# Kernel tuning notes

Hardware: AMD Instinct MI355X
Metric: run time of the kernel (lower is better)

Reference implementation:

```python
import jax, jax.numpy as jnp
import numpy as np

B, L, D, H, NL = 4, 2048, 128, 4, 2
DH = D // H
FF = 2 * D
EPS_LN = 1e-5


def _p(key, shape, scale=0.05):
    return (jax.random.normal(key, shape, dtype=jnp.float32) * scale)


def setup_inputs() -> dict:
    key = jax.random.key(0)
    ks = jax.random.split(key, 40)
    inp = {
        "local_global": jax.random.normal(ks[0], (B, D), dtype=jnp.float32),
        "task_features": jax.random.normal(ks[1], (B, L, 15), dtype=jnp.float32),
        "privacy_features": jax.random.normal(ks[2], (B, L, 6), dtype=jnp.float32),
        "dag_features": jax.random.normal(ks[3], (B, L, 4), dtype=jnp.float32),
        # float mask in [0,1); values > 0.5 are MASKED (set to -inf) per torch code
        "attn_mask": jax.random.uniform(ks[4], (B, L, L), dtype=jnp.float32),
        # input projections (stored [in, out]; torch Linear does x @ W.T + b)
        "task_W": _p(ks[5], (15, D)), "task_b": jnp.zeros((D,), jnp.float32),
        "priv_W": _p(ks[6], (6, D)), "priv_b": jnp.zeros((D,), jnp.float32),
        "dag_W": _p(ks[7], (4, D)), "dag_b": jnp.zeros((D,), jnp.float32),
        "pre_g": jnp.ones((D,), jnp.float32), "pre_b": jnp.zeros((D,), jnp.float32),
        "post_g": jnp.ones((D,), jnp.float32), "post_b": jnp.zeros((D,), jnp.float32),
        "out_W": _p(ks[8], (D, D)), "out_b": jnp.zeros((D,), jnp.float32),
        # per-layer params stacked on leading NL axis
        "qW": _p(ks[9], (NL, D, D)), "qb": jnp.zeros((NL, D), jnp.float32),
        "kW": _p(ks[10], (NL, D, D)), "kb": jnp.zeros((NL, D), jnp.float32),
        "vW": _p(ks[11], (NL, D, D)), "vb": jnp.zeros((NL, D), jnp.float32),
        "oW": _p(ks[12], (NL, D, D)), "ob": jnp.zeros((NL, D), jnp.float32),
        "n1g": jnp.ones((NL, D), jnp.float32), "n1b": jnp.zeros((NL, D), jnp.float32),
        "n2g": jnp.ones((NL, D), jnp.float32), "n2b": jnp.zeros((NL, D), jnp.float32),
        "f1W": _p(ks[13], (NL, D, FF)), "f1b": jnp.zeros((NL, FF), jnp.float32),
        "f2W": _p(ks[14], (NL, FF, D)), "f2b": jnp.zeros((NL, D), jnp.float32),
    }
    return inp


def _layernorm(x, g, b):
    mu = x.mean(-1, keepdims=True)
    var = ((x - mu) ** 2).mean(-1, keepdims=True)
    return (x - mu) * jax.lax.rsqrt(var + EPS_LN) * g + b


def _attention(x, add_mask, Wq, bq, Wk, bk, Wv, bv, Wo, bo):
    # x: [B,L,D]; add_mask: [B,L,L] additive (0 or -inf)
    def heads(y):
        return y.reshape(B, L, H, DH).transpose(0, 2, 1, 3)  # [B,H,L,DH]
    q = heads(x @ Wq + bq)
    k = heads(x @ Wk + bk)
    v = heads(x @ Wv + bv)
    scale = 1.0 / np.sqrt(DH).astype(np.float32)
    scores = jnp.einsum('bhqd,bhkd->bhqk', q, k) * scale + add_mask[:, None]
    # fully-masked-row diagonal fixup (torch: set diag score to 0 where row max is -inf)
    row_max = scores.max(-1)                       # [B,H,L]
    fully_masked = jnp.isinf(row_max) & (row_max < 0)
    eye = jnp.eye(L, dtype=bool)
    scores = jnp.where(fully_masked[..., None] & eye, 0.0, scores)
    w = jax.nn.softmax(scores, axis=-1)
    # NaN fallback: if any NaN, replace with 1/L and renormalize (applied globally, as torch does)
    has_nan = jnp.isnan(w).any()
    fixed = jnp.nan_to_num(w, nan=1.0 / L)
    fixed = fixed / (fixed.sum(-1, keepdims=True) + 1e-8)
    w = jnp.where(has_nan, fixed, w)
    out = jnp.einsum('bhqk,bhkd->bhqd', w, v)      # [B,H,L,DH]
    out = out.transpose(0, 2, 1, 3).reshape(B, L, D)
    return out @ Wo + bo


def reference(local_global, task_features, privacy_features, dag_features, attn_mask,
              task_W, task_b, priv_W, priv_b, dag_W, dag_b,
              pre_g, pre_b, post_g, post_b, out_W, out_b,
              qW, qb, kW, kb, vW, vb, oW, ob,
              n1g, n1b, n2g, n2b, f1W, f1b, f2W, f2b):
    # normalize mask: >0.5 means masked; fix all-False rows by masking their diagonal (torch quirk)
    mb = attn_mask > 0.5                            # [B,L,L] bool, True = mask out
    need_fix = ~mb.any(-1)                          # [B,L]
    eye = jnp.eye(L, dtype=bool)
    mb = mb | (need_fix[..., None] & eye)
    add_mask = jnp.where(mb, -jnp.inf, 0.0).astype(jnp.float32)

    ctx = (task_features @ task_W + task_b) + (privacy_features @ priv_W + priv_b) \
          + (dag_features @ dag_W + dag_b)
    x = _layernorm(ctx, pre_g, pre_b)
    for i in range(NL):  # eval mode: dropout = identity
        sa = _attention(_layernorm(x, n1g[i], n1b[i]), add_mask,
                        qW[i], qb[i], kW[i], kb[i], vW[i], vb[i], oW[i], ob[i])
        x = x + sa
        h = _layernorm(x, n2g[i], n2b[i])
        ff = jax.nn.gelu(h @ f1W[i] + f1b[i], approximate=False) @ f2W[i] + f2b[i]
        x = x + ff
    enc = _layernorm(x, post_g, post_b)
    global_ctx = enc.mean(axis=1)                   # [B,D]
    fused = global_ctx + 0.1 * local_global
    aligned = fused @ out_W + out_b
    return aligned
```

## Files before the change

kernel.cpp:

```cpp
#include <hip/hip_runtime.h>
#include <hip/hip_bf16.h>

#define DEV __device__ __forceinline__

typedef float f32x4 __attribute__((ext_vector_type(4)));
typedef float f32x16 __attribute__((ext_vector_type(16)));
typedef short s16x8 __attribute__((ext_vector_type(8)));
typedef __bf16 bf16x8 __attribute__((ext_vector_type(8)));

DEV bf16x8 as_bf16(s16x8 v) { return __builtin_bit_cast(bf16x8, v); }

DEV unsigned short f2bf(float f) {
    union { __hip_bfloat16 h; unsigned short u; } c;
    c.h = __float2bfloat16(f);
    return c.u;
}

DEV unsigned f2bf2(float lo, float hi) {
    unsigned ulo = __builtin_bit_cast(unsigned, lo);
    unsigned uhi = __builtin_bit_cast(unsigned, hi);
    ulo = (ulo + 0x7fffu + ((ulo >> 16) & 1u)) >> 16;
    uhi = (uhi + 0x7fffu + ((uhi >> 16) & 1u)) & 0xffff0000u;
    return ulo | uhi;
}

DEV float wave_sum64(float v) {
#pragma unroll
    for (int m = 1; m < 64; m <<= 1) v += __shfl_xor(v, m, 64);
    return v;
}

DEV int swz8(int row) { return ((row ^ (row >> 3)) & 7) << 4; }

constexpr float QSCL = (float)(1.4426950408889634 / 5.656854249492381);

__global__ __launch_bounds__(256) void gace_mask_k(
    const float* __restrict__ am, unsigned long long* __restrict__ bits)
{
    const int tid = threadIdx.x, wid = tid >> 6, l = tid & 63;
    const int row = blockIdx.x * 4 + wid;
    const float* mrow = am + (size_t)row * 2048;
    unsigned long long myword = 0, orAll = 0, andAll = ~0ull;
#pragma unroll 4
    for (int w = 0; w < 32; ++w) {
        unsigned long long bal = __ballot(mrow[w * 64 + l] > 0.5f);
        if (w == l) myword = bal;
        orAll |= bal; andAll &= bal;
    }
    const int lrow = row & 2047;
    const int dw = lrow >> 6, dbit = lrow & 63;
    if (l == dw) {
        if (orAll == 0ull) myword |= (1ull << dbit);
        else if (andAll == ~0ull) myword &= ~(1ull << dbit);
    }
    if (l < 32) bits[(size_t)row * 32 + l] = myword;
}

__global__ __launch_bounds__(256) void gace_prep_k(
    const float* __restrict__ qW, const float* __restrict__ kW,
    const float* __restrict__ vW, const float* __restrict__ oW,
    const float* __restrict__ f1W, const float* __restrict__ f2W,
    const float* __restrict__ qb, const float* __restrict__ kb,
    const float* __restrict__ vb,
    unsigned short* __restrict__ wbf, float* __restrict__ bcat)
{
    const int y = blockIdx.y;
    const int idx = blockIdx.x * 256 + threadIdx.x;
    if (y == 6) {
        if (idx < 2 * 384) {
            const int i = idx / 384, j = idx % 384;
            float v;
            if (j < 128)      v = qb[i * 128 + j] * QSCL;
            else if (j < 256) v = kb[i * 128 + j - 128];
            else              v = vb[i * 128 + j - 256];
            bcat[idx] = v;
        }
        return;
    }
    const float* src; int K_, N_, off; float scl = 1.0f;
    switch (y) {
        case 0:  src = qW;  K_ = 128; N_ = 128; off = 0;      scl = QSCL; break;
        case 1:  src = kW;  K_ = 128; N_ = 128; off = 16384;  break;
        case 2:  src = vW;  K_ = 128; N_ = 128; off = 32768;  break;
        case 3:  src = oW;  K_ = 128; N_ = 128; off = 49152;  break;
        case 4:  src = f1W; K_ = 128; N_ = 256; off = 65536;  break;
        default: src = f2W; K_ = 256; N_ = 128; off = 98304;  break;
    }
    const int per = K_ * N_;
    if (idx >= 2 * per) return;
    const int i = idx / per, rem = idx % per;
    const int n = rem / K_, k = rem % K_;
    wbf[(size_t)i * 131072 + off + n * K_ + k] = f2bf(src[(size_t)i * per + k * N_ + n] * scl);
}

__global__ __launch_bounds__(256) void gace_ctxln_k(
    const float* __restrict__ task, const float* __restrict__ priv, const float* __restrict__ dag,
    const float* __restrict__ tW, const float* __restrict__ tb,
    const float* __restrict__ pW, const float* __restrict__ pb,
    const float* __restrict__ dW, const float* __restrict__ db,
    const float* __restrict__ gam, const float* __restrict__ bet,
    float* __restrict__ x)
{
    const int tid = threadIdx.x, wid = tid >> 6, l = tid & 63;
    const int row = blockIdx.x * 4 + wid;
    const int d0 = l, d1 = l + 64;
    float a0 = tb[d0] + pb[d0] + db[d0];
    float a1 = tb[d1] + pb[d1] + db[d1];
    const float* tf = task + (size_t)row * 15;
#pragma unroll
    for (int j = 0; j < 15; ++j) { const float t = tf[j]; a0 += t * tW[j * 128 + d0]; a1 += t * tW[j * 128 + d1]; }
    const float* pf = priv + (size_t)row * 6;
#pragma unroll
    for (int j = 0; j < 6; ++j) { const float t = pf[j]; a0 += t * pW[j * 128 + d0]; a1 += t * pW[j * 128 + d1]; }
    const float* df = dag + (size_t)row * 4;
#pragma unroll
    for (int j = 0; j < 4; ++j) { const float t = df[j]; a0 += t * dW[j * 128 + d0]; a1 += t * dW[j * 128 + d1]; }
    const float s = wave_sum64(a0 + a1);
    const float mean = s * (1.f / 128.f);
    const float e0 = a0 - mean, e1 = a1 - mean;
    const float s2 = wave_sum64(e0 * e0 + e1 * e1);
    const float rs = rsqrtf(s2 * (1.f / 128.f) + 1e-5f);
    x[(size_t)row * 128 + d0] = e0 * rs * gam[d0] + bet[d0];
    x[(size_t)row * 128 + d1] = e1 * rs * gam[d1] + bet[d1];
}

template<int PRO, int EPI, int KD>
__global__ __launch_bounds__(256) void gace_mega_k(
    const unsigned short* __restrict__ A, int lda,
    const float* __restrict__ xin,
    const float* __restrict__ Op, const float* __restrict__ ml,
    const float* __restrict__ gam, const float* __restrict__ bet,
    const unsigned short* __restrict__ Wt,
    const float* __restrict__ bias,
    unsigned short* __restrict__ outb, int ldo,
    float* __restrict__ xadd)
{
    const int tid = threadIdx.x;
    const int wid = tid >> 6, l = tid & 63;
    const int g = (l >> 4) & 3, c16 = l & 15;
    const int m0 = blockIdx.x * 64 + wid * 16;
    const int n0 = blockIdx.y * 64;
    const int arow = m0 + c16;
    constexpr int NKC = KD / 32;

    s16x8 af[NKC];
    if (PRO == 0) {
#pragma unroll
        for (int kc = 0; kc < NKC; ++kc)
            af[kc] = *(const s16x8*)&A[(size_t)arow * lda + kc * 32 + 8 * g];
    } else if (PRO == 1) {
        float v[4][8];
#pragma unroll
        for (int kc = 0; kc < 4; ++kc) {
            const f32x4 a0 = *(const f32x4*)&xin[(size_t)arow * 128 + kc * 32 + 8 * g];
            const f32x4 a1 = *(const f32x4*)&xin[(size_t)arow * 128 + kc * 32 + 8 * g + 4];
#pragma unroll
            for (int e = 0; e < 4; ++e) { v[kc][e] = a0[e]; v[kc][4 + e] = a1[e]; }
        }
        float s = 0.f;
#pragma unroll
        for (int kc = 0; kc < 4; ++kc)
#pragma unroll
            for (int e = 0; e < 8; ++e) s += v[kc][e];
        s += __shfl_xor(s, 16, 64); s += __shfl_xor(s, 32, 64);
        const float mean = s * (1.f / 128.f);
        float s2 = 0.f;
#pragma unroll
        for (int kc = 0; kc < 4; ++kc)
#pragma unroll
            for (int e = 0; e < 8; ++e) { const float d = v[kc][e] - mean; s2 += d * d; }
        s2 += __shfl_xor(s2, 16, 64); s2 += __shfl_xor(s2, 32, 64);
        const float rs = rsqrtf(s2 * (1.f / 128.f) + 1e-5f);
#pragma unroll
        for (int kc = 0; kc < 4; ++kc) {
            union { s16x8 v8; unsigned d[4]; } pk;
#pragma unroll
            for (int j = 0; j < 4; ++j) {
                const int col = kc * 32 + 8 * g + 2 * j;
                const float x0 = (v[kc][2 * j] - mean) * rs * gam[col] + bet[col];
                const float x1 = (v[kc][2 * j + 1] - mean) * rs * gam[col + 1] + bet[col + 1];
                pk.d[j] = f2bf2(x0, x1);
            }
            af[kc] = pk.v8;
        }
    } else {
#pragma unroll
        for (int kc = 0; kc < 4; ++kc) {
            float o[8];
#pragma unroll
            for (int e = 0; e < 8; ++e) o[e] = 0.f;
            float Ls = 0.f;
#pragma unroll
            for (int sp = 0; sp < 4; ++sp) {
                const size_t ro = (size_t)sp * 8192 + arow;
                const f32x4 a0 = *(const f32x4*)&Op[ro * 128 + kc * 32 + 8 * g];
                const f32x4 a1 = *(const f32x4*)&Op[ro * 128 + kc * 32 + 8 * g + 4];
#pragma unroll
                for (int e = 0; e < 4; ++e) { o[e] += a0[e]; o[4 + e] += a1[e]; }
                Ls += ml[ro * 4 + kc];
            }
            const float inv = 1.f / Ls;
            union { s16x8 v8; unsigned d[4]; } pk;
#pragma unroll
            for (int j = 0; j < 4; ++j) pk.d[j] = f2bf2(o[2 * j] * inv, o[2 * j + 1] * inv);
            af[kc] = pk.v8;
        }
    }

    f32x4 acc[4];
#pragma unroll
    for (int i = 0; i < 4; ++i) acc[i] = f32x4{0.f, 0.f, 0.f, 0.f};
#pragma unroll
    for (int ns = 0; ns < 4; ++ns) {
        const unsigned short* wrow = Wt + (size_t)(n0 + 16 * ns + c16) * KD;
#pragma unroll
        for (int kc = 0; kc < NKC; ++kc) {
            const s16x8 bfv = *(const s16x8*)&wrow[kc * 32 + 8 * g];
            acc[ns] = __builtin_amdgcn_mfma_f32_16x16x32_bf16(
                as_bf16(af[kc]), as_bf16(bfv), acc[ns], 0, 0, 0);
        }
    }
#pragma unroll
    for (int ns = 0; ns < 4; ++ns) {
        const int n = n0 + ns * 16 + c16;
        const float bv = bias[n];
#pragma unroll
        for (int r = 0; r < 4; ++r) {
            const int row = m0 + 4 * g + r;
            float v = acc[ns][r] + bv;
            if (EPI == 1) v = v * 0.5f * (1.0f + erff(v * 0.70710678118654752f));
            if (EPI == 2) xadd[(size_t)row * 128 + n] += v;
            else          outb[(size_t)row * ldo + n] = f2bf(v);
        }
    }
}

__global__ __launch_bounds__(256) void gace_flash4_k(
    const unsigned short* __restrict__ QKV,
    const unsigned long long* __restrict__ bits,
    float* __restrict__ Op, float* __restrict__ ml)
{
    __shared__ __align__(16) unsigned short Ks[64 * 40];
    __shared__ __align__(16) char VtB[32 * 128];

    const int tid = threadIdx.x;
    const int wid = tid >> 6, l = tid & 63;
    const int c32 = l & 31, hi = l >> 5;
    const int bid = blockIdx.x;
    const int split = bid & 3, qc = (bid >> 2) & 15, h = (bid >> 6) & 3, b = bid >> 8;
    const size_t base = (size_t)b * 2048;
    const int qb0 = qc * 128 + wid * 32;
    const int q = qb0 + c32;

    const unsigned short* qrow = &QKV[(base + q) * 384 + h * 32];
    const s16x8 qf0 = *(const s16x8*)&qrow[8 * hi];
    const s16x8 qf1 = *(const s16x8*)&qrow[16 + 8 * hi];

    f32x16 oacc, zv;
#pragma unroll
    for (int i = 0; i < 16; ++i) { oacc[i] = 0.f; zv[i] = 0.f; }
    float l_ = 0.f;

    const int sr = tid >> 2;
    const int se = (tid & 3) << 3;
    const int lowr = sr & 31, t12 = lowr & 12;
    const int prow = (sr & 32) | (((t12 == 4) | (t12 == 8)) ? (lowr ^ 12) : lowr);
    unsigned short* kdst = &Ks[prow * 40 + se];
    int voff[8];
#pragma unroll
    for (int j = 0; j < 8; ++j) {
        const int row = se + j;
        voff[j] = row * 128 + ((2 * sr) ^ swz8(row));
    }
    const int vswz = swz8(c32);
    const unsigned short* kbase = &QKV[base * 384 + 128 + h * 32 + se];
    const unsigned short* vbase = kbase + 128;
    const unsigned long long* bq = &bits[(base + q) * 32 + split * 8];

    const int kv0 = split * 512;
    s16x8 kreg = *(const s16x8*)&kbase[(size_t)(kv0 + sr) * 384];
    s16x8 vreg = *(const s16x8*)&vbase[(size_t)(kv0 + sr) * 384];
    unsigned long long wb = bq[0];
    *(s16x8*)kdst = kreg;
    {
        union { s16x8 v; unsigned short u[8]; } vv; vv.v = vreg;
#pragma unroll
        for (int j = 0; j < 8; ++j) *(unsigned short*)&VtB[voff[j]] = vv.u[j];
    }
    __syncthreads();

    for (int t = 0; t < 8; ++t) {
        unsigned long long wbn = 0;
        if (t < 7) {
            const int kvn = kv0 + (t + 1) * 64;
            kreg = *(const s16x8*)&kbase[(size_t)(kvn + sr) * 384];
            vreg = *(const s16x8*)&vbase[(size_t)(kvn + sr) * 384];
            wbn = bq[t + 1];
        }
        const unsigned long long wbs = wb >> (8 * hi);
        const unsigned wlo = (unsigned)wbs, whiw = (unsigned)(wbs >> 32);
#pragma unroll
        for (int H = 0; H < 2; ++H) {
            const unsigned short* krow = &Ks[(32 * H + c32) * 40 + 8 * hi];
            f32x16 sac = __builtin_amdgcn_mfma_f32_32x32x16_bf16(
                as_bf16(*(const s16x8*)&krow[0]), as_bf16(qf0), zv, 0, 0, 0);
            sac = __builtin_amdgcn_mfma_f32_32x32x16_bf16(
                as_bf16(*(const s16x8*)&krow[16]), as_bf16(qf1), sac, 0, 0, 0);
            const unsigned word = (H == 0) ? wlo : whiw;
#pragma unroll
            for (int ch = 0; ch < 2; ++ch) {
                const int c = 2 * H + ch;
                const int bb = ch * 16;
                float p[8];
#pragma unroll
                for (int e = 0; e < 8; ++e) {
                    const float pe = exp2f(sac[ch * 8 + e]);
                    p[e] = ((word >> (bb + e)) & 1u) ? 0.f : pe;
                }
                l_ += ((p[0] + p[1]) + (p[2] + p[3])) + ((p[4] + p[5]) + (p[6] + p[7]));
                union { s16x8 v; unsigned d[4]; } pa;
#pragma unroll
                for (int j = 0; j < 4; ++j)
                    asm("v_cvt_pk_bf16_f32 %0, %1, %2"
                        : "=v"(pa.d[j]) : "v"(p[2 * j]), "v"(p[2 * j + 1]));
                const s16x8 vf = *(const s16x8*)&VtB[c32 * 128 + ((32 * c + 16 * hi) ^ vswz)];
                oacc = __builtin_amdgcn_mfma_f32_32x32x16_bf16(
                    as_bf16(pa.v), as_bf16(vf), oacc, 0, 0, 0);
            }
        }
        if (t < 7) {
            __syncthreads();
            *(s16x8*)kdst = kreg;
            union { s16x8 v; unsigned short u[8]; } vv; vv.v = vreg;
#pragma unroll
            for (int j = 0; j < 8; ++j) *(unsigned short*)&VtB[voff[j]] = vv.u[j];
            __syncthreads();
            wb = wbn;
        }
    }
    l_ += __shfl_xor(l_, 32, 64);
    float* orow = &Op[((size_t)split * 8192 + base + qb0) * 128 + h * 32 + c32];
#pragma unroll
    for (int r = 0; r < 16; ++r) {
        const int qoff = (r & 3) + 8 * (r >> 2) + 4 * hi;
        orow[(size_t)qoff * 128] = oacc[r];
    }
    if (l < 32) ml[((size_t)split * 8192 + base + q) * 4 + h] = l_;
}

__global__ __launch_bounds__(256) void gace_tailA_k(
    const float* __restrict__ x, const float* __restrict__ gam, const float* __restrict__ bet,
    float* __restrict__ partial)
{
    const int tid = threadIdx.x, wid = tid >> 6, l = tid & 63;
    const int row0 = blockIdx.x * 64 + wid * 16;
    const float g0 = gam[l], g1v = gam[l + 64], b0 = bet[l], b1 = bet[l + 64];
    float a0 = 0.f, a1 = 0.f;
    for (int rr = 0; rr < 16; ++rr) {
        const float* xr = x + (size_t)(row0 + rr) * 128;
        const float v0 = xr[l], v1 = xr[l + 64];
        const float s = wave_sum64(v0 + v1);
        const float mean = s * (1.f / 128.f);
        const float d0 = v0 - mean, d1 = v1 - mean;
        const float s2 = wave_sum64(d0 * d0 + d1 * d1);
        const float rs = rsqrtf(s2 * (1.f / 128.f) + 1e-5f);
        a0 += d0 * rs * g0 + b0;
        a1 += d1 * rs * g1v + b1;
    }
    __shared__ float red[4][128];
    red[wid][l] = a0;
    red[wid][l + 64] = a1;
    __syncthreads();
    if (tid < 128) {
        partial[(size_t)blockIdx.x * 128 + tid] =
            red[0][tid] + red[1][tid] + red[2][tid] + red[3][tid];
    }
}

__global__ __launch_bounds__(128) void gace_tailB_k(
    const float* __restrict__ partial, const float* __restrict__ lg,
    const float* __restrict__ oW, const float* __restrict__ obv,
    float* __restrict__ out)
{
    const int tid = threadIdx.x;
    __shared__ float fused[4][128];
#pragma unroll
    for (int b2 = 0; b2 < 4; ++b2) {
        float s = 0.f;
        for (int c = 0; c < 32; ++c) s += partial[(size_t)(b2 * 32 + c) * 128 + tid];
        fused[b2][tid] = s * (1.f / 2048.f) + 0.1f * lg[b2 * 128 + tid];
    }
    __syncthreads();
#pragma unroll
    for (int b2 = 0; b2 < 4; ++b2) {
        float r = obv[tid];
        for (int d2 = 0; d2 < 128; ++d2) r += fused[b2][d2] * oW[d2 * 128 + tid];
        out[b2 * 128 + tid] = r;
    }
}

extern "C" void kernel_launch(void* const* d_in, const int* in_sizes, int n_in,
                              void* d_out, int out_size, void* d_ws, size_t ws_size,
                              hipStream_t stream)
{
    (void)in_sizes; (void)n_in; (void)out_size; (void)ws_size;
    const float* local_global = (const float*)d_in[0];
    const float* task   = (const float*)d_in[1];
    const float* priv   = (const float*)d_in[2];
    const float* dag    = (const float*)d_in[3];
    const float* amask  = (const float*)d_in[4];
    const float* task_W = (const float*)d_in[5];
    const float* task_b = (const float*)d_in[6];
    const float* priv_W = (const float*)d_in[7];
    const float* priv_b = (const float*)d_in[8];
    const float* dag_W  = (const float*)d_in[9];
    const float* dag_b  = (const float*)d_in[10];
    const float* pre_g  = (const float*)d_in[11];
    const float* pre_b  = (const float*)d_in[12];
    const float* post_g = (const float*)d_in[13];
    const float* post_b = (const float*)d_in[14];
    const float* out_W  = (const float*)d_in[15];
    const float* out_b  = (const float*)d_in[16];
    const float* qW = (const float*)d_in[17];
    const float* qb = (const float*)d_in[18];
    const float* kW = (const float*)d_in[19];
    const float* kb = (const float*)d_in[20];
    const float* vW = (const float*)d_in[21];
    const float* vb = (const float*)d_in[22];
    const float* oW = (const float*)d_in[23];
    const float* ob = (const float*)d_in[24];
    const float* n1g = (const float*)d_in[25];
    const float* n1b = (const float*)d_in[26];
    const float* n2g = (const float*)d_in[27];
    const float* n2b = (const float*)d_in[28];
    const float* f1W = (const float*)d_in[29];
    const float* f1b = (const float*)d_in[30];
    const float* f2W = (const float*)d_in[31];
    const float* f2b = (const float*)d_in[32];

    char* ws = (char*)d_ws;
    size_t off = 0;
    auto carve = [&](size_t sz) {
        void* p = ws + off;
        off += (sz + 255) & ~(size_t)255;
        return p;
    };
    unsigned long long* bits = (unsigned long long*)carve(8192ull * 32 * 8);
    float*          x    = (float*)carve(8192ull * 128 * 4);
    unsigned short* qkv  = (unsigned short*)carve(8192ull * 384 * 2);
    unsigned short* g1   = (unsigned short*)carve(8192ull * 256 * 2);
    float*          part = (float*)carve(128ull * 128 * 4);
    float*          Op   = (float*)carve(4ull * 8192 * 128 * 4);
    float*          mlb  = (float*)carve(4ull * 8192 * 4 * 4);
    unsigned short* wbf  = (unsigned short*)carve(2ull * 131072 * 2);
    float*          bcat = (float*)carve(2ull * 384 * 4);

    gace_prep_k<<<dim3(256, 7), 256, 0, stream>>>(qW, kW, vW, oW, f1W, f2W,
                                                  qb, kb, vb, wbf, bcat);
    gace_mask_k<<<2048, 256, 0, stream>>>(amask, bits);
    gace_ctxln_k<<<2048, 256, 0, stream>>>(task, priv, dag, task_W, task_b,
                                           priv_W, priv_b, dag_W, dag_b,
                                           pre_g, pre_b, x);
    for (int i = 0; i < 2; ++i) {
        const unsigned short* wl = wbf + (size_t)i * 131072;
        gace_mega_k<1, 0, 128><<<dim3(128, 6), 256, 0, stream>>>(
            nullptr, 0, x, nullptr, nullptr, n1g + i * 128, n1b + i * 128,
            wl, bcat + i * 384, qkv, 384, nullptr);
        gace_flash4_k<<<1024, 256, 0, stream>>>(qkv, bits, Op, mlb);
        gace_mega_k<2, 2, 128><<<dim3(128, 2), 256, 0, stream>>>(
            nullptr, 0, nullptr, Op, mlb, nullptr, nullptr,
            wl + 49152, ob + i * 128, nullptr, 0, x);
        gace_mega_k<1, 1, 128><<<dim3(128, 4), 256, 0, stream>>>(
            nullptr, 0, x, nullptr, nullptr, n2g + i * 128, n2b + i * 128,
            wl + 65536, f1b + i * 256, g1, 256, nullptr);
        gace_mega_k<0, 2, 256><<<dim3(128, 2), 256, 0, stream>>>(
            g1, 256, nullptr, nullptr, nullptr, nullptr, nullptr,
            wl + 98304, f2b + i * 128, nullptr, 0, x);
    }
    gace_tailA_k<<<128, 256, 0, stream>>>(x, post_g, post_b, part);
    gace_tailB_k<<<1, 128, 0, stream>>>(part, local_global, out_W, out_b, (float*)d_out);
}
```

Measured before the change: 189.1 us.

## Write V transposed from QKV GEMM and drop LDS staging in flash attention

The QKV projection epilogue now writes V in a transposed [head_dim, token] layout and Q/K into a narrower buffer. The flash attention kernel then reads K and V fragments straight from global memory, with no LDS staging and no per-tile barriers. The mask, context-layernorm and weight-prep kernels are also merged into a single launch to cut launch overhead. The risk is that direct global loads of K/V per wave, without shared-memory reuse, may add memory traffic and latency that the removed barriers do not make up for.

```diff
diff --git a/kernel.cpp b/kernel.cpp
--- a/kernel.cpp
+++ b/kernel.cpp
@@ -6,6 +6,7 @@
 typedef float f32x4 __attribute__((ext_vector_type(4)));
 typedef float f32x16 __attribute__((ext_vector_type(16)));
 typedef short s16x8 __attribute__((ext_vector_type(8)));
+typedef unsigned short u16x4 __attribute__((ext_vector_type(4)));
 typedef __bf16 bf16x8 __attribute__((ext_vector_type(8)));
 
 DEV bf16x8 as_bf16(s16x8 v) { return __builtin_bit_cast(bf16x8, v); }
@@ -30,33 +31,16 @@
     return v;
 }
 
-DEV int swz8(int row) { return ((row ^ (row >> 3)) & 7) << 4; }
-
 constexpr float QSCL = (float)(1.4426950408889634 / 5.656854249492381);
 
-__global__ __launch_bounds__(256) void gace_mask_k(
-    const float* __restrict__ am, unsigned long long* __restrict__ bits)
-{
-    const int tid = threadIdx.x, wid = tid >> 6, l = tid & 63;
-    const int row = blockIdx.x * 4 + wid;
-    const float* mrow = am + (size_t)row * 2048;
-    unsigned long long myword = 0, orAll = 0, andAll = ~0ull;
-#pragma unroll 4
-    for (int w = 0; w < 32; ++w) {
-        unsigned long long bal = __ballot(mrow[w * 64 + l] > 0.5f);
-        if (w == l) myword = bal;
-        orAll |= bal; andAll &= bal;
-    }
-    const int lrow = row & 2047;
-    const int dw = lrow >> 6, dbit = lrow & 63;
-    if (l == dw) {
-        if (orAll == 0ull) myword |= (1ull << dbit);
-        else if (andAll == ~0ull) myword &= ~(1ull << dbit);
-    }
-    if (l < 32) bits[(size_t)row * 32 + l] = myword;
-}
-
-__global__ __launch_bounds__(256) void gace_prep_k(
+__global__ __launch_bounds__(256) void gace_setup_k(
+    const float* __restrict__ am, unsigned long long* __restrict__ bits,
+    const float* __restrict__ task, const float* __restrict__ priv, const float* __restrict__ dag,
+    const float* __restrict__ tW, const float* __restrict__ tb,
+    const float* __restrict__ pW, const float* __restrict__ pb,
+    const float* __restrict__ dW, const float* __restrict__ db,
+    const float* __restrict__ pre_g, const float* __restrict__ pre_b,
+    float* __restrict__ x,
     const float* __restrict__ qW, const float* __restrict__ kW,
     const float* __restrict__ vW, const float* __restrict__ oW,
     const float* __restrict__ f1W, const float* __restrict__ f2W,
@@ -64,8 +48,53 @@
     const float* __restrict__ vb,
     unsigned short* __restrict__ wbf, float* __restrict__ bcat)
 {
-    const int y = blockIdx.y;
-    const int idx = blockIdx.x * 256 + threadIdx.x;
+    const int bx = blockIdx.x;
+    const int tid = threadIdx.x, wid = tid >> 6, l = tid & 63;
+    if (bx < 2048) {
+        const int row = bx * 4 + wid;
+        const float* mrow = am + (size_t)row * 2048;
+        unsigned long long myword = 0, orAll = 0, andAll = ~0ull;
+#pragma unroll 4
+        for (int w = 0; w < 32; ++w) {
+            unsigned long long bal = __ballot(mrow[w * 64 + l] > 0.5f);
+            if (w == l) myword = bal;
+            orAll |= bal; andAll &= bal;
+        }
+        const int lrow = row & 2047;
+        const int dw = lrow >> 6, dbit = lrow & 63;
+        if (l == dw) {
+            if (orAll == 0ull) myword |= (1ull << dbit);
+            else if (andAll == ~0ull) myword &= ~(1ull << dbit);
+        }
+        if (l < 32) bits[(size_t)row * 32 + l] = myword;
+        return;
+    }
+    if (bx < 4096) {
+        const int row = (bx - 2048) * 4 + wid;
+        const int d0 = l, d1 = l + 64;
+        float a0 = tb[d0] + pb[d0] + db[d0];
+        float a1 = tb[d1] + pb[d1] + db[d1];
+        const float* tf = task + (size_t)row * 15;
+#pragma unroll
+        for (int j = 0; j < 15; ++j) { const float t = tf[j]; a0 += t * tW[j * 128 + d0]; a1 += t * tW[j * 128 + d1]; }
+        const float* pf = priv + (size_t)row * 6;
+#pragma unroll
+        for (int j = 0; j < 6; ++j) { const float t = pf[j]; a0 += t * pW[j * 128 + d0]; a1 += t * pW[j * 128 + d1]; }
+        const float* df = dag + (size_t)row * 4;
+#pragma unroll
+        for (int j = 0; j < 4; ++j) { const float t = df[j]; a0 += t * dW[j * 128 + d0]; a1 += t * dW[j * 128 + d1]; }
+        const float s = wave_sum64(a0 + a1);
+        const float mean = s * (1.f / 128.f);
+        const float e0 = a0 - mean, e1 = a1 - mean;
+        const float s2 = wave_sum64(e0 * e0 + e1 * e1);
+        const float rs = rsqrtf(s2 * (1.f / 128.f) + 1e-5f);
+        x[(size_t)row * 128 + d0] = e0 * rs * pre_g[d0] + pre_b[d0];
+        x[(size_t)row * 128 + d1] = e1 * rs * pre_g[d1] + pre_b[d1];
+        return;
+    }
+    const int bx2 = bx - 4096;
+    const int y = bx2 >> 8;
+    const int idx = (bx2 & 255) * 256 + tid;
     if (y == 6) {
         if (idx < 2 * 384) {
             const int i = idx / 384, j = idx % 384;
@@ -91,37 +120,6 @@
     const int i = idx / per, rem = idx % per;
     const int n = rem / K_, k = rem % K_;
     wbf[(size_t)i * 131072 + off + n * K_ + k] = f2bf(src[(size_t)i * per + k * N_ + n] * scl);
-}
-
-__global__ __launch_bounds__(256) void gace_ctxln_k(
-    const float* __restrict__ task, const float* __restrict__ priv, const float* __restrict__ dag,
-    const float* __restrict__ tW, const float* __restrict__ tb,
-    const float* __restrict__ pW, const float* __restrict__ pb,
-    const float* __restrict__ dW, const float* __restrict__ db,
-    const float* __restrict__ gam, const float* __restrict__ bet,
-    float* __restrict__ x)
-{
-    const int tid = threadIdx.x, wid = tid >> 6, l = tid & 63;
-    const int row = blockIdx.x * 4 + wid;
-    const int d0 = l, d1 = l + 64;
-    float a0 = tb[d0] + pb[d0] + db[d0];
-    float a1 = tb[d1] + pb[d1] + db[d1];
-    const float* tf = task + (size_t)row * 15;
-#pragma unroll
-    for (int j = 0; j < 15; ++j) { const float t = tf[j]; a0 += t * tW[j * 128 + d0]; a1 += t * tW[j * 128 + d1]; }
-    const float* pf = priv + (size_t)row * 6;
-#pragma unroll
-    for (int j = 0; j < 6; ++j) { const float t = pf[j]; a0 += t * pW[j * 128 + d0]; a1 += t * pW[j * 128 + d1]; }
-    const float* df = dag + (size_t)row * 4;
-#pragma unroll
-    for (int j = 0; j < 4; ++j) { const float t = df[j]; a0 += t * dW[j * 128 + d0]; a1 += t * dW[j * 128 + d1]; }
-    const float s = wave_sum64(a0 + a1);
-    const float mean = s * (1.f / 128.f);
-    const float e0 = a0 - mean, e1 = a1 - mean;
-    const float s2 = wave_sum64(e0 * e0 + e1 * e1);
-    const float rs = rsqrtf(s2 * (1.f / 128.f) + 1e-5f);
-    x[(size_t)row * 128 + d0] = e0 * rs * gam[d0] + bet[d0];
-    x[(size_t)row * 128 + d1] = e1 * rs * gam[d1] + bet[d1];
 }
 
 template<int PRO, int EPI, int KD>
@@ -133,7 +131,7 @@
     const unsigned short* __restrict__ Wt,
     const float* __restrict__ bias,
     unsigned short* __restrict__ outb, int ldo,
-    float* __restrict__ xadd)
+    float* __restrict__ xadd, unsigned short* __restrict__ vtbuf)
 {
     const int tid = threadIdx.x;
     const int wid = tid >> 6, l = tid & 63;
@@ -220,6 +218,19 @@
                 as_bf16(af[kc]), as_bf16(bfv), acc[ns], 0, 0, 0);
         }
     }
+    if (EPI == 0 && vtbuf != nullptr && n0 >= 256) {
+        const int row0 = m0 + 4 * g;
+#pragma unroll
+        for (int ns = 0; ns < 4; ++ns) {
+            const int n = n0 + ns * 16 + c16;
+            const float bv = bias[n];
+            u16x4 pk;
+#pragma unroll
+            for (int r = 0; r < 4; ++r) pk[r] = f2bf(acc[ns][r] + bv);
+            *(u16x4*)&vtbuf[(size_t)(n - 256) * 8192 + row0] = pk;
+        }
+        return;
+    }
 #pragma unroll
     for (int ns = 0; ns < 4; ++ns) {
         const int n = n0 + ns * 16 + c16;
@@ -235,14 +246,12 @@
     }
 }
 
-__global__ __launch_bounds__(256) void gace_flash4_k(
-    const unsigned short* __restrict__ QKV,
+__global__ __launch_bounds__(256) void gace_flash5_k(
+    const unsigned short* __restrict__ QK,
+    const unsigned short* __restrict__ Vt,
     const unsigned long long* __restrict__ bits,
     float* __restrict__ Op, float* __restrict__ ml)
 {
-    __shared__ __align__(16) unsigned short Ks[64 * 40];
-    __shared__ __align__(16) char VtB[32 * 128];
-
     const int tid = threadIdx.x;
     const int wid = tid >> 6, l = tid & 63;
     const int c32 = l & 31, hi = l >> 5;
@@ -252,60 +261,33 @@
     const int qb0 = qc * 128 + wid * 32;
     const int q = qb0 + c32;
 
-    const unsigned short* qrow = &QKV[(base + q) * 384 + h * 32];
+    const unsigned short* qrow = &QK[(base + q) * 256 + h * 32];
     const s16x8 qf0 = *(const s16x8*)&qrow[8 * hi];
     const s16x8 qf1 = *(const s16x8*)&qrow[16 + 8 * hi];
 
+    const int t12 = c32 & 12;
+    const int kvA = (t12 == 4 || t12 == 8) ? (c32 ^ 12) : c32;
+
     f32x16 oacc, zv;
 #pragma unroll
     for (int i = 0; i < 16; ++i) { oacc[i] = 0.f; zv[i] = 0.f; }
     float l_ = 0.f;
 
-    const int sr = tid >> 2;
-    const int se = (tid & 3) << 3;
-    const int lowr = sr & 31, t12 = lowr & 12;
-    const int prow = (sr & 32) | (((t12 == 4) | (t12 == 8)) ? (lowr ^ 12) : lowr);
-    unsigned short* kdst = &Ks[prow * 40 + se];
-    int voff[8];
-#pragma unroll
-    for (int j = 0; j < 8; ++j) {
-        const int row = se + j;
-        voff[j] = row * 128 + ((2 * sr) ^ swz8(row));
-    }
-    const int vswz = swz8(c32);
-    const unsigned short* kbase = &QKV[base * 384 + 128 + h * 32 + se];
-    const unsigned short* vbase = kbase + 128;
+    const int kv0 = split * 512;
     const unsigned long long* bq = &bits[(base + q) * 32 + split * 8];
-
-    const int kv0 = split * 512;
-    s16x8 kreg = *(const s16x8*)&kbase[(size_t)(kv0 + sr) * 384];
-    s16x8 vreg = *(const s16x8*)&vbase[(size_t)(kv0 + sr) * 384];
-    unsigned long long wb = bq[0];
-    *(s16x8*)kdst = kreg;
-    {
-        union { s16x8 v; unsigned short u[8]; } vv; vv.v = vreg;
-#pragma unroll
-        for (int j = 0; j < 8; ++j) *(unsigned short*)&VtB[voff[j]] = vv.u[j];
-    }
-    __syncthreads();
+    const unsigned short* kbase = &QK[(base + kv0) * 256 + 128 + h * 32 + 8 * hi];
+    const unsigned short* vtb = &Vt[(size_t)(h * 32 + c32) * 8192 + base + kv0 + 8 * hi];
 
     for (int t = 0; t < 8; ++t) {
-        unsigned long long wbn = 0;
-        if (t < 7) {
-            const int kvn = kv0 + (t + 1) * 64;
-            kreg = *(const s16x8*)&kbase[(size_t)(kvn + sr) * 384];
-            vreg = *(const s16x8*)&vbase[(size_t)(kvn + sr) * 384];
-            wbn = bq[t + 1];
-        }
-        const unsigned long long wbs = wb >> (8 * hi);
+        const unsigned long long wbs = bq[t] >> (8 * hi);
         const unsigned wlo = (unsigned)wbs, whiw = (unsigned)(wbs >> 32);
 #pragma unroll
         for (int H = 0; H < 2; ++H) {
-            const unsigned short* krow = &Ks[(32 * H + c32) * 40 + 8 * hi];
+            const unsigned short* kr = kbase + (size_t)(t * 64 + 32 * H + kvA) * 256;
             f32x16 sac = __builtin_amdgcn_mfma_f32_32x32x16_bf16(
-                as_bf16(*(const s16x8*)&krow[0]), as_bf16(qf0), zv, 0, 0, 0);
+                as_bf16(*(const s16x8*)&kr[0]), as_bf16(qf0), zv, 0, 0, 0);
             sac = __builtin_amdgcn_mfma_f32_32x32x16_bf16(
-                as_bf16(*(const s16x8*)&krow[16]), as_bf16(qf1), sac, 0, 0, 0);
+                as_bf16(*(const s16x8*)&kr[16]), as_bf16(qf1), sac, 0, 0, 0);
             const unsigned word = (H == 0) ? wlo : whiw;
 #pragma unroll
             for (int ch = 0; ch < 2; ++ch) {
@@ -323,19 +305,10 @@
                 for (int j = 0; j < 4; ++j)
                     asm("v_cvt_pk_bf16_f32 %0, %1, %2"
                         : "=v"(pa.d[j]) : "v"(p[2 * j]), "v"(p[2 * j + 1]));
-                const s16x8 vf = *(const s16x8*)&VtB[c32 * 128 + ((32 * c + 16 * hi) ^ vswz)];
+                const s16x8 vf = *(const s16x8*)&vtb[t * 64 + 16 * c];
                 oacc = __builtin_amdgcn_mfma_f32_32x32x16_bf16(
                     as_bf16(pa.v), as_bf16(vf), oacc, 0, 0, 0);
             }
-        }
-        if (t < 7) {
-            __syncthreads();
-            *(s16x8*)kdst = kreg;
-            union { s16x8 v; unsigned short u[8]; } vv; vv.v = vreg;
-#pragma unroll
-            for (int j = 0; j < 8; ++j) *(unsigned short*)&VtB[voff[j]] = vv.u[j];
-            __syncthreads();
-            wb = wbn;
         }
     }
     l_ += __shfl_xor(l_, 32, 64);
@@ -447,7 +420,8 @@
     };
     unsigned long long* bits = (unsigned long long*)carve(8192ull * 32 * 8);
     float*          x    = (float*)carve(8192ull * 128 * 4);
-    unsigned short* qkv  = (unsigned short*)carve(8192ull * 384 * 2);
+    unsigned short* qk   = (unsigned short*)carve(8192ull * 256 * 2);
+    unsigned short* vt   = (unsigned short*)carve(128ull * 8192 * 2);
     unsigned short* g1   = (unsigned short*)carve(8192ull * 256 * 2);
     float*          part = (float*)carve(128ull * 128 * 4);
     float*          Op   = (float*)carve(4ull * 8192 * 128 * 4);
@@ -455,27 +429,26 @@
     unsigned short* wbf  = (unsigned short*)carve(2ull * 131072 * 2);
     float*          bcat = (float*)carve(2ull * 384 * 4);
 
-    gace_prep_k<<<dim3(256, 7), 256, 0, stream>>>(qW, kW, vW, oW, f1W, f2W,
-                                                  qb, kb, vb, wbf, bcat);
-    gace_mask_k<<<2048, 256, 0, stream>>>(amask, bits);
-    gace_ctxln_k<<<2048, 256, 0, stream>>>(task, priv, dag, task_W, task_b,
-                                           priv_W, priv_b, dag_W, dag_b,
-                                           pre_g, pre_b, x);
+    gace_setup_k<<<5888, 256, 0, stream>>>(
+        amask, bits,
+        task, priv, dag, task_W, task_b, priv_W, priv_b, dag_W, dag_b,
+        pre_g, pre_b, x,
+        qW, kW, vW, oW, f1W, f2W, qb, kb, vb, wbf, bcat);
     for (int i = 0; i < 2; ++i) {
         const unsigned short* wl = wbf + (size_t)i * 131072;
         gace_mega_k<1, 0, 128><<<dim3(128, 6), 256, 0, stream>>>(
             nullptr, 0, x, nullptr, nullptr, n1g + i * 128, n1b + i * 128,
-            wl, bcat + i * 384, qkv, 384, nullptr);
-        gace_flash4_k<<<1024, 256, 0, stream>>>(qkv, bits, Op, mlb);
+            wl, bcat + i * 384, qk, 256, nullptr, vt);
+        gace_flash5_k<<<1024, 256, 0, stream>>>(qk, vt, bits, Op, mlb);
         gace_mega_k<2, 2, 128><<<dim3(128, 2), 256, 0, stream>>>(
             nullptr, 0, nullptr, Op, mlb, nullptr, nullptr,
-            wl + 49152, ob + i * 128, nullptr, 0, x);
+            wl + 49152, ob + i * 128, nullptr, 0, x, nullptr);
         gace_mega_k<1, 1, 128><<<dim3(128, 4), 256, 0, stream>>>(
             nullptr, 0, x, nullptr, nullptr, n2g + i * 128, n2b + i * 128,
-            wl + 65536, f1b + i * 256, g1, 256, nullptr);
+            wl + 65536, f1b + i * 256, g1, 256, nullptr, nullptr);
         gace_mega_k<0, 2, 256><<<dim3(128, 2), 256, 0, stream>>>(
             g1, 256, nullptr, nullptr, nullptr, nullptr, nullptr,
-            wl + 98304, f2b + i * 128, nullptr, 0, x);
+            wl + 98304, f2b + i * 128, nullptr, 0, x, nullptr);
     }
     gace_tailA_k<<<128, 256, 0, stream>>>(x, post_g, post_b, part);
     gace_tailB_k<<<1, 128, 0, stream>>>(part, local_global, out_W, out_b, (float*)d_out);
```

Measured after the change: 201.7 us. 6.6% more time.
